# Kernel optimization log

Measured on AMD Instinct MI355X. Metric: run time of the kernel, lower is better.

Reference implementation:

```python
import jax, jax.numpy as jnp
import numpy as np

OCC_SIZE = (200, 200, 16)  # n_query = 640000
N_CAM, C, H, W = 6, 128, 64, 176


def setup_inputs() -> dict:
    key = jax.random.key(0)
    k1, k2, k3 = jax.random.split(key, 3)
    n_query = OCC_SIZE[0] * OCC_SIZE[1] * OCC_SIZE[2]
    img_feats = jax.random.normal(k1, (N_CAM, C, H, W), dtype=jnp.float32)
    # pixel coords: x in [0, W-1], y in [0, H-1] (in-range, as the torch code assumes)
    uv = jax.random.uniform(k2, (N_CAM, n_query, 2), dtype=jnp.float32)
    points = uv * jnp.array([W - 1, H - 1], dtype=jnp.float32)
    valid = jax.random.bernoulli(k3, 0.3, (N_CAM, n_query))
    return {"img_feats": img_feats, "points": points, "valid": valid}


def reference(img_feats, points, valid):
    # Faithful to fast_voxel_fill: sequential per-camera masked writes mean the
    n_cam, n_channels = img_feats.shape[0], img_feats.shape[1]
    n_query = points.shape[-2]
    x = jnp.round(points[..., 0]).astype(jnp.int32)  # [n_cam, n_query] -> W index
    y = jnp.round(points[..., 1]).astype(jnp.int32)  # [n_cam, n_query] -> H index
    cam_ids = jnp.arange(n_cam, dtype=jnp.int32)[:, None]
    sel = jnp.max(jnp.where(valid, cam_ids, -1), axis=0)  # [n_query], -1 = no valid cam
    any_valid = sel >= 0
    cam = jnp.maximum(sel, 0)
    q = jnp.arange(n_query)
    xs = x[cam, q]
    ys = y[cam, q]
    gathered = img_feats[cam, :, ys, xs]  # [n_query, C]
    volume = jnp.where(any_valid[:, None], gathered, 0.0).T  # [C, n_query]
    return volume.reshape(n_channels, OCC_SIZE[0], OCC_SIZE[1], OCC_SIZE[2])
```

## Files before the change

### kernel.cpp

```cpp
#include <hip/hip_runtime.h>

#define NCAM 6
#define CCH  128
#define IH   64
#define IW   176
#define NQ   640000
#define PIX  (IH * IW)

__global__ __launch_bounds__(256) void transpose_kernel(
    const float* __restrict__ in, float* __restrict__ out) {
    __shared__ float tile[32][33];
    const int cam   = blockIdx.z;
    const int pbase = blockIdx.x * 32;
    const int cbase = blockIdx.y * 32;
    const int tx = threadIdx.x, ty = threadIdx.y;

    const float* src = in  + (size_t)cam * CCH * PIX;
    float*       dst = out + (size_t)cam * PIX * CCH;

    #pragma unroll
    for (int j = 0; j < 4; ++j) {
        int c = cbase + ty + j * 8;
        tile[ty + j * 8][tx] = src[(size_t)c * PIX + (pbase + tx)];
    }
    __syncthreads();
    #pragma unroll
    for (int j = 0; j < 4; ++j) {
        int p = pbase + ty + j * 8;
        dst[(size_t)p * CCH + (cbase + tx)] = tile[tx][ty + j * 8];
    }
}

__global__ __launch_bounds__(256) void gather_kernel(
    const float* __restrict__ imgT,
    const float* __restrict__ points,
    const int*   __restrict__ valid,
    float*       __restrict__ out) {
    const int q = blockIdx.x * 256 + threadIdx.x;

    int sel = -1;
    #pragma unroll
    for (int cam = 0; cam < NCAM; ++cam)
        if (valid[(size_t)cam * NQ + q] != 0) sel = cam;

    const float scale = (sel >= 0) ? 1.0f : 0.0f;
    const int cam = (sel >= 0) ? sel : 0;

    const float2 pt = ((const float2*)points)[(size_t)cam * NQ + q];
    const int x = __float2int_rn(pt.x);
    const int y = __float2int_rn(pt.y);

    const float4* src =
        (const float4*)(imgT + (((size_t)cam * IH + y) * IW + x) * CCH);

    #pragma unroll 8
    for (int c4 = 0; c4 < CCH / 4; ++c4) {
        float4 v = src[c4];
        out[(size_t)(c4 * 4 + 0) * NQ + q] = v.x * scale;
        out[(size_t)(c4 * 4 + 1) * NQ + q] = v.y * scale;
        out[(size_t)(c4 * 4 + 2) * NQ + q] = v.z * scale;
        out[(size_t)(c4 * 4 + 3) * NQ + q] = v.w * scale;
    }
}

__global__ __launch_bounds__(256) void gather_direct_kernel(
    const float* __restrict__ img,
    const float* __restrict__ points,
    const int*   __restrict__ valid,
    float*       __restrict__ out) {
    const int q = blockIdx.x * 256 + threadIdx.x;

    int sel = -1;
    #pragma unroll
    for (int cam = 0; cam < NCAM; ++cam)
        if (valid[(size_t)cam * NQ + q] != 0) sel = cam;

    const float scale = (sel >= 0) ? 1.0f : 0.0f;
    const int cam = (sel >= 0) ? sel : 0;

    const float2 pt = ((const float2*)points)[(size_t)cam * NQ + q];
    const int x = __float2int_rn(pt.x);
    const int y = __float2int_rn(pt.y);

    const float* src = img + ((size_t)cam * CCH * IH + y) * IW + x;
    #pragma unroll 8
    for (int c = 0; c < CCH; ++c)
        out[(size_t)c * NQ + q] = src[(size_t)c * PIX] * scale;
}

extern "C" void kernel_launch(void* const* d_in, const int* in_sizes, int n_in,
                              void* d_out, int out_size, void* d_ws, size_t ws_size,
                              hipStream_t stream) {
    const float* img    = (const float*)d_in[0];
    const float* points = (const float*)d_in[1];
    const int*   valid  = (const int*)  d_in[2];
    float*       out    = (float*)d_out;

    const size_t need = (size_t)NCAM * CCH * IH * IW * sizeof(float);
    if (ws_size >= need) {
        float* imgT = (float*)d_ws;
        dim3 tb(32, 8, 1);
        dim3 tg(PIX / 32, CCH / 32, NCAM);
        transpose_kernel<<<tg, tb, 0, stream>>>(img, imgT);
        gather_kernel<<<NQ / 256, 256, 0, stream>>>(imgT, points, valid, out);
    } else {
        gather_direct_kernel<<<NQ / 256, 256, 0, stream>>>(img, points, valid, out);
    }
}
```

Before: 452.6 us.

## Stage gathered features through LDS to emit wide coalesced output stores

Reworks the gather kernel so each block handles 64 queries. One pass resolves the winning camera and base offset per query into shared memory. Groups of 32 lanes then read a full 128-channel row with float4 loads and stage it in a padded LDS tile, and the block writes the output transposed as float4 stores along the query dimension. This targets the many scalar, poorly vectorized output stores of the old one-thread-per-query layout, at the cost of about 33KB of LDS per block, two barriers, and only a quarter of the threads active during the setup phase.

Result: faster. 432.5 us (-4.4%).

```diff
diff --git a/kernel.cpp b/kernel.cpp
--- a/kernel.cpp
+++ b/kernel.cpp
@@ -6,6 +6,8 @@
 #define IW   176
 #define NQ   640000
 #define PIX  (IH * IW)
+#define QT   64
+#define LSTRIDE 129
 
 __global__ __launch_bounds__(256) void transpose_kernel(
     const float* __restrict__ in, float* __restrict__ out) {
@@ -31,35 +33,66 @@
     }
 }
 
-__global__ __launch_bounds__(256) void gather_kernel(
+__global__ __launch_bounds__(256) void gather_lds_kernel(
     const float* __restrict__ imgT,
     const float* __restrict__ points,
     const int*   __restrict__ valid,
     float*       __restrict__ out) {
-    const int q = blockIdx.x * 256 + threadIdx.x;
+    __shared__ float feat[QT * LSTRIDE];
+    __shared__ int   sbase[QT];
+    __shared__ float sscale[QT];
 
-    int sel = -1;
-    #pragma unroll
-    for (int cam = 0; cam < NCAM; ++cam)
-        if (valid[(size_t)cam * NQ + q] != 0) sel = cam;
+    const int t     = threadIdx.x;
+    const int qbase = blockIdx.x * QT;
 
-    const float scale = (sel >= 0) ? 1.0f : 0.0f;
-    const int cam = (sel >= 0) ? sel : 0;
+    if (t < QT) {
+        const int q = qbase + t;
+        int sel = -1;
+        #pragma unroll
+        for (int cam = 0; cam < NCAM; ++cam)
+            if (valid[(size_t)cam * NQ + q] != 0) sel = cam;
+        const int cam = (sel >= 0) ? sel : 0;
+        sscale[t] = (sel >= 0) ? 1.0f : 0.0f;
+        const float2 pt = ((const float2*)points)[(size_t)cam * NQ + q];
+        const int x = __float2int_rn(pt.x);
+        const int y = __float2int_rn(pt.y);
+        sbase[t] = ((cam * IH + y) * IW + x) * CCH;
+    }
+    __syncthreads();
 
-    const float2 pt = ((const float2*)points)[(size_t)cam * NQ + q];
-    const int x = __float2int_rn(pt.x);
-    const int y = __float2int_rn(pt.y);
+    {
+        const int grp  = t >> 5;
+        const int lane = t & 31;
+        #pragma unroll
+        for (int i = 0; i < 8; ++i) {
+            const int ql = i * 8 + grp;
+            const float s = sscale[ql];
+            const float4 v = *((const float4*)(imgT + sbase[ql]) + lane);
+            const int w = ql * LSTRIDE + 4 * lane;
+            feat[w + 0] = v.x * s;
+            feat[w + 1] = v.y * s;
+            feat[w + 2] = v.z * s;
+            feat[w + 3] = v.w * s;
+        }
+    }
+    __syncthreads();
 
-    const float4* src =
-        (const float4*)(imgT + (((size_t)cam * IH + y) * IW + x) * CCH);
-
-    #pragma unroll 8
-    for (int c4 = 0; c4 < CCH / 4; ++c4) {
-        float4 v = src[c4];
-        out[(size_t)(c4 * 4 + 0) * NQ + q] = v.x * scale;
-        out[(size_t)(c4 * 4 + 1) * NQ + q] = v.y * scale;
-        out[(size_t)(c4 * 4 + 2) * NQ + q] = v.z * scale;
-        out[(size_t)(c4 * 4 + 3) * NQ + q] = v.w * scale;
+    {
+        const int l    = t & 63;
+        const int wv   = t >> 6;
+        const int qq   = l & 15;
+        const int csub = l >> 4;
+        #pragma unroll
+        for (int iter = 0; iter < 8; ++iter) {
+            const int c    = iter * 16 + wv * 4 + csub;
+            const int qoff = 4 * qq;
+            float4 v;
+            v.x = feat[(qoff + 0) * LSTRIDE + c];
+            v.y = feat[(qoff + 1) * LSTRIDE + c];
+            v.z = feat[(qoff + 2) * LSTRIDE + c];
+            v.w = feat[(qoff + 3) * LSTRIDE + c];
+            *(float4*)(out + (size_t)c * NQ + qbase + qoff) = v;
+        }
     }
 }
 
@@ -102,7 +135,7 @@
         dim3 tb(32, 8, 1);
         dim3 tg(PIX / 32, CCH / 32, NCAM);
         transpose_kernel<<<tg, tb, 0, stream>>>(img, imgT);
-        gather_kernel<<<NQ / 256, 256, 0, stream>>>(imgT, points, valid, out);
+        gather_lds_kernel<<<NQ / QT, 256, 0, stream>>>(imgT, points, valid, out);
     } else {
         gather_direct_kernel<<<NQ / 256, 256, 0, stream>>>(img, points, valid, out);
     }
```

## Stage per-wave gathered features in LDS for coalesced reads and vector stores

Applied to the files above, without the earlier changes.

Replaces the one-thread-per-query gather with a persistent kernel in which each wave handles 16 queries. Half-waves read each query's 128-channel feature row contiguously into padded shared memory. The wave then writes channel-major output as float4 stores of 4 consecutive queries. This targets the scattered per-thread row reads and the scalar strided stores of the old kernel. In exchange, each channel row now gets only 64-byte contiguous output segments, and the code relies on wave-lockstep execution instead of a barrier between shared-memory writes and reads.

New measurement: 502.2 us. 10.9% more time.

```diff
diff --git a/kernel.cpp b/kernel.cpp
--- a/kernel.cpp
+++ b/kernel.cpp
@@ -6,6 +6,7 @@
 #define IW   176
 #define NQ   640000
 #define PIX  (IH * IW)
+#define LSTR 132
 
 __global__ __launch_bounds__(256) void transpose_kernel(
     const float* __restrict__ in, float* __restrict__ out) {
@@ -31,35 +32,60 @@
     }
 }
 
-__global__ __launch_bounds__(256) void gather_kernel(
+__global__ __launch_bounds__(256) void gather_wave_kernel(
     const float* __restrict__ imgT,
     const float* __restrict__ points,
     const int*   __restrict__ valid,
-    float*       __restrict__ out) {
-    const int q = blockIdx.x * 256 + threadIdx.x;
+    float*       __restrict__ out,
+    int n_tiles) {
+    __shared__ float feat[4][16 * LSTR];
+    __shared__ int   sbase_s[4][16];
+    __shared__ float sscale_s[4][16];
 
-    int sel = -1;
-    #pragma unroll
-    for (int cam = 0; cam < NCAM; ++cam)
-        if (valid[(size_t)cam * NQ + q] != 0) sel = cam;
+    const int t    = threadIdx.x;
+    const int wv   = t >> 6;
+    const int l    = t & 63;
+    const int half = l >> 5;
+    const int hl   = l & 31;
+    const int qq   = l & 3;
+    const int csub = l >> 2;
 
-    const float scale = (sel >= 0) ? 1.0f : 0.0f;
-    const int cam = (sel >= 0) ? sel : 0;
+    for (int tile = blockIdx.x; tile < n_tiles; tile += gridDim.x) {
+        const int qbase = tile * 64 + wv * 16;
 
-    const float2 pt = ((const float2*)points)[(size_t)cam * NQ + q];
-    const int x = __float2int_rn(pt.x);
-    const int y = __float2int_rn(pt.y);
+        if (l < 16) {
+            const int q = qbase + l;
+            int sel = -1;
+            #pragma unroll
+            for (int cam = 0; cam < NCAM; ++cam)
+                if (valid[(size_t)cam * NQ + q] != 0) sel = cam;
+            const int cam = (sel >= 0) ? sel : 0;
+            sscale_s[wv][l] = (sel >= 0) ? 1.0f : 0.0f;
+            const float2 pt = ((const float2*)points)[(size_t)cam * NQ + q];
+            const int x = __float2int_rn(pt.x);
+            const int y = __float2int_rn(pt.y);
+            sbase_s[wv][l] = ((cam * IH + y) * IW + x) * CCH;
+        }
 
-    const float4* src =
-        (const float4*)(imgT + (((size_t)cam * IH + y) * IW + x) * CCH);
+        #pragma unroll
+        for (int i = 0; i < 8; ++i) {
+            const int   ql = i * 2 + half;
+            const float s  = sscale_s[wv][ql];
+            const float4 v = *((const float4*)(imgT + sbase_s[wv][ql]) + hl);
+            float4* w = (float4*)&feat[wv][ql * LSTR + 4 * hl];
+            *w = make_float4(v.x * s, v.y * s, v.z * s, v.w * s);
+        }
 
-    #pragma unroll 8
-    for (int c4 = 0; c4 < CCH / 4; ++c4) {
-        float4 v = src[c4];
-        out[(size_t)(c4 * 4 + 0) * NQ + q] = v.x * scale;
-        out[(size_t)(c4 * 4 + 1) * NQ + q] = v.y * scale;
-        out[(size_t)(c4 * 4 + 2) * NQ + q] = v.z * scale;
-        out[(size_t)(c4 * 4 + 3) * NQ + q] = v.w * scale;
+        #pragma unroll
+        for (int it = 0; it < 8; ++it) {
+            const int c = it * 16 + csub;
+            float4 v;
+            v.x = feat[wv][(4 * qq + 0) * LSTR + c];
+            v.y = feat[wv][(4 * qq + 1) * LSTR + c];
+            v.z = feat[wv][(4 * qq + 2) * LSTR + c];
+            v.w = feat[wv][(4 * qq + 3) * LSTR + c];
+            *(float4*)(out + (size_t)c * NQ + qbase + 4 * qq) = v;
+        }
     }
 }
 
@@ -102,7 +128,8 @@
         dim3 tb(32, 8, 1);
         dim3 tg(PIX / 32, CCH / 32, NCAM);
         transpose_kernel<<<tg, tb, 0, stream>>>(img, imgT);
-        gather_kernel<<<NQ / 256, 256, 0, stream>>>(imgT, points, valid, out);
+        gather_wave_kernel<<<2048, 256, 0, stream>>>(imgT, points, valid, out,
+                                                     NQ / 64);
     } else {
         gather_direct_kernel<<<NQ / 256, 256, 0, stream>>>(img, points, valid, out);
     }
```
